# Optimization experiments

Measured on AMD Instinct MI355X. Metric: run time of the kernel, lower is better.

The kernel has to match this reference:

```python
import jax, jax.numpy as jnp
import numpy as np

ETA = 0.01
EPSILON = 1e-08


def setup_inputs() -> dict:
    key = jax.random.key(0)
    k1, k2 = jax.random.split(key)
    B, N = 2000000, 16  # batch (time steps), num_assets
    weights = jax.random.uniform(k1, (B, N), dtype=jnp.float32)
    next_returns = jax.random.normal(k2, (B, N), dtype=jnp.float32) * 0.02
    return {"weights": weights, "next_returns": next_returns}


def reference(weights, next_returns):
    # portfolio return per time step: (B,)
    R = jnp.sum(weights * next_returns, axis=1)
    batch_size = R.shape[0]
    eta = jnp.asarray(ETA, R.dtype)
    eps = jnp.asarray(EPSILON, R.dtype)

    def step(carry, R_t):
        A_prev, B_prev = carry
        delta_A = eta * (R_t - A_prev)
        delta_B = eta * (R_t * R_t - B_prev)
        variance = jnp.maximum(B_prev - A_prev * A_prev, eps)
        denom = variance ** 1.5
        D_t = (B_prev * delta_A - 0.5 * A_prev * delta_B) / denom
        return (A_prev + delta_A, B_prev + delta_B), D_t

    init = (jnp.asarray(0.0, R.dtype), jnp.asarray(EPSILON, R.dtype))
    _, D = jax.lax.scan(step, init, R)
    return -jnp.sum(D) / batch_size
```

## Files before the change

kernel.cpp:

```cpp
#include <hip/hip_runtime.h>


#define D_ETA 0.01
#define D_C   (1.0 - D_ETA)
#define D_EPS 1e-8

constexpr int BLOCK = 256;
constexpr int CHUNK = 2048;
constexpr int LPT   = CHUNK / BLOCK;
constexpr int GRP   = CHUNK / 64;

#define SCOPE __HIP_MEMORY_SCOPE_AGENT

__device__ __forceinline__ int pidx(int i) { return i + (i >> 3); }
constexpr int RS_SIZE = CHUNK + CHUNK / 8;

__device__ __forceinline__ double dot4d(float4 a, float4 b) {
    return (double)a.x * (double)b.x + (double)a.y * (double)b.y
         + (double)a.z * (double)b.z + (double)a.w * (double)b.w;
}

__device__ __forceinline__ float row_R(const float* __restrict__ w,
                                       const float* __restrict__ x,
                                       long long row) {
    const float4* w4 = (const float4*)(w + row * 16);
    const float4* x4 = (const float4*)(x + row * 16);
    double r = 0.0;
#pragma unroll
    for (int q = 0; q < 4; ++q) r += dot4d(w4[q], x4[q]);
    return (float)r;
}

__device__ __forceinline__ void wave_combine(double& m, double& a, double& b) {
    int lane = threadIdx.x & 63;
#pragma unroll
    for (int off = 1; off < 64; off <<= 1) {
        double pm = __shfl_down(m, off, 64);
        double pa = __shfl_down(a, off, 64);
        double pb = __shfl_down(b, off, 64);
        if (lane + off < 64) {
            a = pm * a + pa;
            b = pm * b + pb;
            m = pm * m;
        }
    }
}

__device__ __forceinline__ void block_scan(double& m, double& sA, double& sB,
                                           double* mS, double* aS, double* bS) {
    int tid = threadIdx.x;
    mS[tid] = m; aS[tid] = sA; bS[tid] = sB;
    __syncthreads();
#pragma unroll
    for (int off = 1; off < BLOCK; off <<= 1) {
        double pm = 1.0, pa = 0.0, pb = 0.0;
        if (tid >= off) { pm = mS[tid - off]; pa = aS[tid - off]; pb = bS[tid - off]; }
        __syncthreads();
        if (tid >= off) {
            sA = m * pa + sA;
            sB = m * pb + sB;
            m  = pm * m;
        }
        mS[tid] = m; aS[tid] = sA; bS[tid] = sB;
        __syncthreads();
    }
}

__global__ __launch_bounds__(64) void k0_init(unsigned* __restrict__ ctl)
{
    if (threadIdx.x < 4) ctl[threadIdx.x] = 0u;
}

__global__ __launch_bounds__(BLOCK) void k1_dots_agg(
    const float* __restrict__ w, const float* __restrict__ x, int nrows,
    float* __restrict__ Rws,
    double* __restrict__ aggs)
{
    __shared__ float Rs[RS_SIZE];
    __shared__ double wM[4], wA[4], wB[4];
    int tid = threadIdx.x;
    int q    = tid & 3;
    int rsub = tid >> 2;
    long long base = (long long)blockIdx.x * CHUNK;
    const float4* w4 = (const float4*)w;
    const float4* x4 = (const float4*)x;
    long long f0 = base * 4 + tid;

    if (base + CHUNK <= (long long)nrows) {
#pragma unroll
        for (int g = 0; g < GRP; g += 4) {
            float4 a0 = w4[f0 + (long long)(g + 0) * 256];
            float4 a1 = w4[f0 + (long long)(g + 1) * 256];
            float4 a2 = w4[f0 + (long long)(g + 2) * 256];
            float4 a3 = w4[f0 + (long long)(g + 3) * 256];
            float4 b0 = x4[f0 + (long long)(g + 0) * 256];
            float4 b1 = x4[f0 + (long long)(g + 1) * 256];
            float4 b2 = x4[f0 + (long long)(g + 2) * 256];
            float4 b3 = x4[f0 + (long long)(g + 3) * 256];
            double p0 = dot4d(a0, b0), p1 = dot4d(a1, b1);
            double p2 = dot4d(a2, b2), p3 = dot4d(a3, b3);
            p0 += __shfl_xor(p0, 1, 64); p0 += __shfl_xor(p0, 2, 64);
            p1 += __shfl_xor(p1, 1, 64); p1 += __shfl_xor(p1, 2, 64);
            p2 += __shfl_xor(p2, 1, 64); p2 += __shfl_xor(p2, 2, 64);
            p3 += __shfl_xor(p3, 1, 64); p3 += __shfl_xor(p3, 2, 64);
            if (q == 0) {
                Rs[pidx((g + 0) * 64 + rsub)] = (float)p0;
                Rs[pidx((g + 1) * 64 + rsub)] = (float)p1;
                Rs[pidx((g + 2) * 64 + rsub)] = (float)p2;
                Rs[pidx((g + 3) * 64 + rsub)] = (float)p3;
                if (Rws) {
                    Rws[base + (g + 0) * 64 + rsub] = (float)p0;
                    Rws[base + (g + 1) * 64 + rsub] = (float)p1;
                    Rws[base + (g + 2) * 64 + rsub] = (float)p2;
                    Rws[base + (g + 3) * 64 + rsub] = (float)p3;
                }
            }
        }
    } else {
        for (int g = 0; g < GRP; ++g) {
            long long row = base + g * 64 + rsub;
            double p = 0.0;
            if (row < nrows) p = dot4d(w4[row * 4 + q], x4[row * 4 + q]);
            p += __shfl_xor(p, 1, 64);
            p += __shfl_xor(p, 2, 64);
            if (q == 0) {
                Rs[pidx(g * 64 + rsub)] = (float)p;
                if (Rws && row < nrows) Rws[row] = (float)p;
            }
        }
    }
    __syncthreads();

    int start = tid * LPT;
    long long rem = (long long)nrows - (base + start);
    int len = rem >= LPT ? LPT : (rem > 0 ? (int)rem : 0);
    double m = 1.0, sA = 0.0, sB = 0.0;
    for (int k = 0; k < len; ++k) {
        double r = (double)Rs[pidx(start + k)];
        sA = D_C * sA + D_ETA * r;
        sB = D_C * sB + D_ETA * (r * r);
        m *= D_C;
    }
    wave_combine(m, sA, sB);
    int wv = tid >> 6;
    if ((tid & 63) == 0) { wM[wv] = m; wA[wv] = sA; wB[wv] = sB; }
    __syncthreads();
    if (tid == 0) {
        double cm = wM[0], ca = wA[0], cb = wB[0];
#pragma unroll
        for (int v = 1; v < 4; ++v) {
            ca = wM[v] * ca + wA[v];
            cb = wM[v] * cb + wB[v];
            cm = wM[v] * cm;
        }
        double* ag = aggs + (size_t)blockIdx.x * 3;
        ag[0] = cm; ag[1] = ca; ag[2] = cb;
    }
}

__global__ __launch_bounds__(BLOCK) void k2_replay(
    const float* __restrict__ Rws,
    const float* __restrict__ w, const float* __restrict__ x, int nrows,
    const double* __restrict__ aggs, int nb,
    double* __restrict__ acc, unsigned* __restrict__ done,
    float* __restrict__ out)
{
    __shared__ double mS[BLOCK], aS[BLOCK], bS[BLOCK];
    __shared__ double exAB[2];
    __shared__ double wsum[BLOCK / 64];
    int tid = threadIdx.x;
    int cid = blockIdx.x;
    long long base = (long long)cid * CHUNK;
    long long g0 = base + (long long)tid * LPT;
    long long rem = (long long)nrows - g0;
    int len = rem >= LPT ? LPT : (rem > 0 ? (int)rem : 0);

    float rv[LPT];
    if (Rws) {
        if (len == LPT) {
            const float4* Rp = (const float4*)(Rws + g0);
            float4 u = Rp[0], v = Rp[1];
            rv[0]=u.x; rv[1]=u.y; rv[2]=u.z; rv[3]=u.w;
            rv[4]=v.x; rv[5]=v.y; rv[6]=v.z; rv[7]=v.w;
        } else {
            for (int k = 0; k < len; ++k) rv[k] = Rws[g0 + k];
        }
    } else {
        for (int k = 0; k < len; ++k) rv[k] = row_R(w, x, g0 + k);
    }

    double m = 1.0, sA = 0.0, sB = 0.0;
    for (int k = 0; k < len; ++k) {
        double r = (double)rv[k];
        sA = D_C * sA + D_ETA * r;
        sB = D_C * sB + D_ETA * (r * r);
        m *= D_C;
    }
    block_scan(m, sA, sB, mS, aS, bS);

    if (tid < 64) {
        int K = (cid + 63) >> 6;
        int lo = tid * K;
        int hi = lo + K; if (hi > cid) hi = cid;
        double pm = 1.0, pa = 0.0, pb = 0.0;
        for (int j = lo; j < hi; ++j) {
            const double* ag = aggs + (size_t)j * 3;
            double jm = ag[0], ja = ag[1], jb = ag[2];
            pa = jm * pa + ja;
            pb = jm * pb + jb;
            pm = jm * pm;
        }
        wave_combine(pm, pa, pb);
        if (tid == 0) {
            exAB[0] = pa;
            exAB[1] = pm * D_EPS + pb;
        }
    }
    __syncthreads();

    double em = 1.0, ea = 0.0, eb = 0.0;
    if (tid > 0) { em = mS[tid - 1]; ea = aS[tid - 1]; eb = bS[tid - 1]; }
    double A = em * exAB[0] + ea;
    double B = em * exAB[1] + eb;

    double dsum = 0.0;
    for (int k = 0; k < len; ++k) {
        double r = (double)rv[k];
        double dA = D_ETA * (r - A);
        double dB = D_ETA * (r * r - B);
        double var = B - A * A;
        if (var < D_EPS) var = D_EPS;
        double denom = var * sqrt(var);
        dsum += (B * dA - 0.5 * A * dB) / denom;
        A += dA;
        B += dB;
    }

#pragma unroll
    for (int off = 32; off > 0; off >>= 1) dsum += __shfl_down(dsum, off, 64);
    if ((tid & 63) == 0) wsum[tid >> 6] = dsum;
    __syncthreads();

    if (tid == 0) {
        double bs = wsum[0] + wsum[1] + wsum[2] + wsum[3];
        __hip_atomic_fetch_add(acc, bs, __ATOMIC_RELAXED, SCOPE);
        unsigned r = __hip_atomic_fetch_add(done, 1u, __ATOMIC_ACQ_REL, SCOPE);
        if (r == (unsigned)(nb - 1)) {
            double total = __hip_atomic_load(acc, __ATOMIC_RELAXED, SCOPE);
            out[0] = (float)(-total / (double)nrows);
        }
    }
}

extern "C" void kernel_launch(void* const* d_in, const int* in_sizes, int n_in,
                              void* d_out, int out_size, void* d_ws, size_t ws_size,
                              hipStream_t stream)
{
    const float* w = (const float*)d_in[0];
    const float* x = (const float*)d_in[1];
    int nrows = in_sizes[0] / 16;
    int nb = (nrows + CHUNK - 1) / CHUNK;

    unsigned* ctl  = (unsigned*)d_ws;
    double*   acc  = (double*)d_ws;
    unsigned* done = ctl + 2;
    double*   aggs = (double*)((char*)d_ws + 64);
    size_t roff = (64 + (size_t)nb * 3 * sizeof(double) + 255) & ~(size_t)255;
    float* Rws = nullptr;
    if (ws_size >= roff + (size_t)nrows * sizeof(float))
        Rws = (float*)((char*)d_ws + roff);

    k0_init<<<1, 64, 0, stream>>>(ctl);
    k1_dots_agg<<<nb, BLOCK, 0, stream>>>(w, x, nrows, Rws, aggs);
    k2_replay<<<nb, BLOCK, 0, stream>>>(Rws, w, x, nrows, aggs, nb,
                                        acc, done, (float*)d_out);
}
```

Before: 311.4 us.

## Fuse dot, scan and replay into one cooperative kernel with grid syncs

```diff
diff --git a/kernel.cpp b/kernel.cpp
--- a/kernel.cpp
+++ b/kernel.cpp
@@ -1,4 +1,7 @@
 #include <hip/hip_runtime.h>
+#include <hip/hip_cooperative_groups.h>
+
+namespace cg = cooperative_groups;
 
 
 #define D_ETA 0.01
@@ -9,6 +12,7 @@
 constexpr int CHUNK = 2048;
 constexpr int LPT   = CHUNK / BLOCK;
 constexpr int GRP   = CHUNK / 64;
+constexpr int MAXNB = 1024;
 
 #define SCOPE __HIP_MEMORY_SCOPE_AGENT
 
@@ -66,22 +70,26 @@
     }
 }
 
-__global__ __launch_bounds__(64) void k0_init(unsigned* __restrict__ ctl)
-{
-    if (threadIdx.x < 4) ctl[threadIdx.x] = 0u;
-}
-
-__global__ __launch_bounds__(BLOCK) void k1_dots_agg(
-    const float* __restrict__ w, const float* __restrict__ x, int nrows,
-    float* __restrict__ Rws,
-    double* __restrict__ aggs)
-{
-    __shared__ float Rs[RS_SIZE];
-    __shared__ double wM[4], wA[4], wB[4];
+__global__ __launch_bounds__(BLOCK) void k_coop(
+    const float* __restrict__ w, const float* __restrict__ x,
+    int nrows, int nb,
+    double* __restrict__ aggs,
+    double* __restrict__ acc,
+    float*  __restrict__ out)
+{
+    __shared__ float  Rs[RS_SIZE];
+    __shared__ double mS[BLOCK], aS[BLOCK], bS[BLOCK];
+    __shared__ double exAB[2];
+    __shared__ double wsum[BLOCK / 64];
+
     int tid = threadIdx.x;
+    int cid = blockIdx.x;
+    long long base = (long long)cid * CHUNK;
+
+    if (cid == 0 && tid == 0) *acc = 0.0;
+
     int q    = tid & 3;
     int rsub = tid >> 2;
-    long long base = (long long)blockIdx.x * CHUNK;
     const float4* w4 = (const float4*)w;
     const float4* x4 = (const float4*)x;
     long long f0 = base * 4 + tid;
@@ -108,12 +116,6 @@
                 Rs[pidx((g + 1) * 64 + rsub)] = (float)p1;
                 Rs[pidx((g + 2) * 64 + rsub)] = (float)p2;
                 Rs[pidx((g + 3) * 64 + rsub)] = (float)p3;
-                if (Rws) {
-                    Rws[base + (g + 0) * 64 + rsub] = (float)p0;
-                    Rws[base + (g + 1) * 64 + rsub] = (float)p1;
-                    Rws[base + (g + 2) * 64 + rsub] = (float)p2;
-                    Rws[base + (g + 3) * 64 + rsub] = (float)p3;
-                }
             }
         }
     } else {
@@ -123,10 +125,7 @@
             if (row < nrows) p = dot4d(w4[row * 4 + q], x4[row * 4 + q]);
             p += __shfl_xor(p, 1, 64);
             p += __shfl_xor(p, 2, 64);
-            if (q == 0) {
-                Rs[pidx(g * 64 + rsub)] = (float)p;
-                if (Rws && row < nrows) Rws[row] = (float)p;
-            }
+            if (q == 0) Rs[pidx(g * 64 + rsub)] = (float)p;
         }
     }
     __syncthreads();
@@ -141,62 +140,14 @@
         sB = D_C * sB + D_ETA * (r * r);
         m *= D_C;
     }
-    wave_combine(m, sA, sB);
-    int wv = tid >> 6;
-    if ((tid & 63) == 0) { wM[wv] = m; wA[wv] = sA; wB[wv] = sB; }
-    __syncthreads();
-    if (tid == 0) {
-        double cm = wM[0], ca = wA[0], cb = wB[0];
-#pragma unroll
-        for (int v = 1; v < 4; ++v) {
-            ca = wM[v] * ca + wA[v];
-            cb = wM[v] * cb + wB[v];
-            cm = wM[v] * cm;
-        }
-        double* ag = aggs + (size_t)blockIdx.x * 3;
-        ag[0] = cm; ag[1] = ca; ag[2] = cb;
-    }
-}
-
-__global__ __launch_bounds__(BLOCK) void k2_replay(
-    const float* __restrict__ Rws,
-    const float* __restrict__ w, const float* __restrict__ x, int nrows,
-    const double* __restrict__ aggs, int nb,
-    double* __restrict__ acc, unsigned* __restrict__ done,
-    float* __restrict__ out)
-{
-    __shared__ double mS[BLOCK], aS[BLOCK], bS[BLOCK];
-    __shared__ double exAB[2];
-    __shared__ double wsum[BLOCK / 64];
-    int tid = threadIdx.x;
-    int cid = blockIdx.x;
-    long long base = (long long)cid * CHUNK;
-    long long g0 = base + (long long)tid * LPT;
-    long long rem = (long long)nrows - g0;
-    int len = rem >= LPT ? LPT : (rem > 0 ? (int)rem : 0);
-
-    float rv[LPT];
-    if (Rws) {
-        if (len == LPT) {
-            const float4* Rp = (const float4*)(Rws + g0);
-            float4 u = Rp[0], v = Rp[1];
-            rv[0]=u.x; rv[1]=u.y; rv[2]=u.z; rv[3]=u.w;
-            rv[4]=v.x; rv[5]=v.y; rv[6]=v.z; rv[7]=v.w;
-        } else {
-            for (int k = 0; k < len; ++k) rv[k] = Rws[g0 + k];
-        }
-    } else {
-        for (int k = 0; k < len; ++k) rv[k] = row_R(w, x, g0 + k);
-    }
-
-    double m = 1.0, sA = 0.0, sB = 0.0;
-    for (int k = 0; k < len; ++k) {
-        double r = (double)rv[k];
-        sA = D_C * sA + D_ETA * r;
-        sB = D_C * sB + D_ETA * (r * r);
-        m *= D_C;
-    }
     block_scan(m, sA, sB, mS, aS, bS);
+    if (tid == BLOCK - 1) {
+        double* ag = aggs + (size_t)cid * 3;
+        ag[0] = m; ag[1] = sA; ag[2] = sB;
+    }
+    __threadfence();
+
+    cg::this_grid().sync();
 
     if (tid < 64) {
         int K = (cid + 63) >> 6;
@@ -225,6 +176,138 @@
 
     double dsum = 0.0;
     for (int k = 0; k < len; ++k) {
+        double r = (double)Rs[pidx(start + k)];
+        double dA = D_ETA * (r - A);
+        double dB = D_ETA * (r * r - B);
+        double var = B - A * A;
+        if (var < D_EPS) var = D_EPS;
+        double denom = var * sqrt(var);
+        dsum += (B * dA - 0.5 * A * dB) / denom;
+        A += dA;
+        B += dB;
+    }
+#pragma unroll
+    for (int off = 32; off > 0; off >>= 1) dsum += __shfl_down(dsum, off, 64);
+    if ((tid & 63) == 0) wsum[tid >> 6] = dsum;
+    __syncthreads();
+    if (tid == 0) {
+        double bs = wsum[0] + wsum[1] + wsum[2] + wsum[3];
+        __hip_atomic_fetch_add(acc, bs, __ATOMIC_RELAXED, SCOPE);
+    }
+
+    cg::this_grid().sync();
+
+    if (cid == 0 && tid == 0)
+        out[0] = (float)(-(*acc) / (double)nrows);
+}
+
+__global__ __launch_bounds__(64) void k0_init(unsigned* __restrict__ ctl)
+{
+    if (threadIdx.x < 4) ctl[threadIdx.x] = 0u;
+}
+
+__global__ __launch_bounds__(BLOCK) void k1_fb(
+    const float* __restrict__ w, const float* __restrict__ x, int nrows,
+    float* __restrict__ Rws, double* __restrict__ aggs)
+{
+    __shared__ float Rs[RS_SIZE];
+    __shared__ double wM[4], wA[4], wB[4];
+    int tid = threadIdx.x;
+    int q = tid & 3, rsub = tid >> 2;
+    long long base = (long long)blockIdx.x * CHUNK;
+    const float4* w4 = (const float4*)w;
+    const float4* x4 = (const float4*)x;
+    for (int g = 0; g < GRP; ++g) {
+        long long row = base + g * 64 + rsub;
+        double p = 0.0;
+        if (row < nrows) p = dot4d(w4[row * 4 + q], x4[row * 4 + q]);
+        p += __shfl_xor(p, 1, 64);
+        p += __shfl_xor(p, 2, 64);
+        if (q == 0) {
+            Rs[pidx(g * 64 + rsub)] = (float)p;
+            if (Rws && row < nrows) Rws[row] = (float)p;
+        }
+    }
+    __syncthreads();
+    int start = tid * LPT;
+    long long rem = (long long)nrows - (base + start);
+    int len = rem >= LPT ? LPT : (rem > 0 ? (int)rem : 0);
+    double m = 1.0, sA = 0.0, sB = 0.0;
+    for (int k = 0; k < len; ++k) {
+        double r = (double)Rs[pidx(start + k)];
+        sA = D_C * sA + D_ETA * r;
+        sB = D_C * sB + D_ETA * (r * r);
+        m *= D_C;
+    }
+    wave_combine(m, sA, sB);
+    int wv = tid >> 6;
+    if ((tid & 63) == 0) { wM[wv] = m; wA[wv] = sA; wB[wv] = sB; }
+    __syncthreads();
+    if (tid == 0) {
+        double cm = wM[0], ca = wA[0], cb = wB[0];
+#pragma unroll
+        for (int v = 1; v < 4; ++v) {
+            ca = wM[v] * ca + wA[v];
+            cb = wM[v] * cb + wB[v];
+            cm = wM[v] * cm;
+        }
+        double* ag = aggs + (size_t)blockIdx.x * 3;
+        ag[0] = cm; ag[1] = ca; ag[2] = cb;
+    }
+}
+
+__global__ __launch_bounds__(BLOCK) void k2_fb(
+    const float* __restrict__ Rws,
+    const float* __restrict__ w, const float* __restrict__ x, int nrows,
+    const double* __restrict__ aggs, int nb,
+    double* __restrict__ acc, unsigned* __restrict__ done,
+    float* __restrict__ out)
+{
+    __shared__ double mS[BLOCK], aS[BLOCK], bS[BLOCK];
+    __shared__ double exAB[2];
+    __shared__ double wsum[BLOCK / 64];
+    int tid = threadIdx.x;
+    int cid = blockIdx.x;
+    long long g0 = (long long)cid * CHUNK + (long long)tid * LPT;
+    long long rem = (long long)nrows - g0;
+    int len = rem >= LPT ? LPT : (rem > 0 ? (int)rem : 0);
+
+    float rv[LPT];
+    if (Rws) {
+        for (int k = 0; k < len; ++k) rv[k] = Rws[g0 + k];
+    } else {
+        for (int k = 0; k < len; ++k) rv[k] = row_R(w, x, g0 + k);
+    }
+    double m = 1.0, sA = 0.0, sB = 0.0;
+    for (int k = 0; k < len; ++k) {
+        double r = (double)rv[k];
+        sA = D_C * sA + D_ETA * r;
+        sB = D_C * sB + D_ETA * (r * r);
+        m *= D_C;
+    }
+    block_scan(m, sA, sB, mS, aS, bS);
+    if (tid < 64) {
+        int K = (cid + 63) >> 6;
+        int lo = tid * K;
+        int hi = lo + K; if (hi > cid) hi = cid;
+        double pm = 1.0, pa = 0.0, pb = 0.0;
+        for (int j = lo; j < hi; ++j) {
+            const double* ag = aggs + (size_t)j * 3;
+            double jm = ag[0], ja = ag[1], jb = ag[2];
+            pa = jm * pa + ja;
+            pb = jm * pb + jb;
+            pm = jm * pm;
+        }
+        wave_combine(pm, pa, pb);
+        if (tid == 0) { exAB[0] = pa; exAB[1] = pm * D_EPS + pb; }
+    }
+    __syncthreads();
+    double em = 1.0, ea = 0.0, eb = 0.0;
+    if (tid > 0) { em = mS[tid - 1]; ea = aS[tid - 1]; eb = bS[tid - 1]; }
+    double A = em * exAB[0] + ea;
+    double B = em * exAB[1] + eb;
+    double dsum = 0.0;
+    for (int k = 0; k < len; ++k) {
         double r = (double)rv[k];
         double dA = D_ETA * (r - A);
         double dB = D_ETA * (r * r - B);
@@ -235,12 +318,10 @@
         A += dA;
         B += dB;
     }
-
 #pragma unroll
     for (int off = 32; off > 0; off >>= 1) dsum += __shfl_down(dsum, off, 64);
     if ((tid & 63) == 0) wsum[tid >> 6] = dsum;
     __syncthreads();
-
     if (tid == 0) {
         double bs = wsum[0] + wsum[1] + wsum[2] + wsum[3];
         __hip_atomic_fetch_add(acc, bs, __ATOMIC_RELAXED, SCOPE);
@@ -270,8 +351,16 @@
     if (ws_size >= roff + (size_t)nrows * sizeof(float))
         Rws = (float*)((char*)d_ws + roff);
 
-    k0_init<<<1, 64, 0, stream>>>(ctl);
-    k1_dots_agg<<<nb, BLOCK, 0, stream>>>(w, x, nrows, Rws, aggs);
-    k2_replay<<<nb, BLOCK, 0, stream>>>(Rws, w, x, nrows, aggs, nb,
+    if (nb <= MAXNB) {
+        float* out = (float*)d_out;
+        void* args[] = { (void*)&w, (void*)&x, (void*)&nrows, (void*)&nb,
+                         (void*)&aggs, (void*)&acc, (void*)&out };
+        hipLaunchCooperativeKernel((const void*)k_coop, dim3(nb), dim3(BLOCK),
+                                   args, 0, stream);
+    } else {
+        k0_init<<<1, 64, 0, stream>>>(ctl);
+        k1_fb<<<nb, BLOCK, 0, stream>>>(w, x, nrows, Rws, aggs);
+        k2_fb<<<nb, BLOCK, 0, stream>>>(Rws, w, x, nrows, aggs, nb,
                                         acc, done, (float*)d_out);
-}
+    }
+}
```

Measured after the change: 622.5 us. +99.9%, slower.
